# Performance work log

Hardware: AMD Instinct MI355X
Metric: run time of the kernel (lower is better)

## Reference

```python
import jax, jax.numpy as jnp
import numpy as np
import math

# dims matching init_kwargs
B, N, CS, CZ = 1, 512, 384, 128
H, C, PQ, PV = 8, 128, 8, 8
INF, EPS = 1e5, 1e-8

# ---- quaternion / motor helpers (PGA motor encoded as [qw,qx,qy,qz,tx,ty,tz,0]) ----

def quat_conj(q):
    return q * jnp.array([1.0, -1.0, -1.0, -1.0], q.dtype)

def quat_mul(a, b):
    aw, ax, ay, az = jnp.split(a, 4, -1)
    bw, bx, by, bz = jnp.split(b, 4, -1)
    return jnp.concatenate([
        aw*bw - ax*bx - ay*by - az*bz,
        aw*bx + ax*bw + ay*bz - az*by,
        aw*by - ax*bz + ay*bw + az*bx,
        aw*bz + ax*by - ay*bx + az*bw], -1)

def quat_rotate(q, v):
    qv = q[..., 1:]
    uv = jnp.cross(qv, v)
    uuv = jnp.cross(qv, uv)
    return v + 2.0 * (q[..., :1] * uv + uuv)

def point_trafo(p, q, t):
    # p [...,K,3]; rigid transform by frame motor, homogeneous 4-vector out
    pp = quat_rotate(q, p) + t
    return jnp.concatenate([pp, jnp.ones_like(pp[..., :1])], -1)

def mv_transform(mv, q, t):
    # versor sandwich on a 16-dim multivector: three rotatable 3-vector blocks,
    # the point block (7:10, weight at 10) also translates; slots 0 and 10:16 invariant
    s0 = mv[..., 0:1]
    v1 = quat_rotate(q, mv[..., 1:4])
    v2 = quat_rotate(q, mv[..., 4:7])
    w = mv[..., 10:11]
    p = quat_rotate(q, mv[..., 7:10]) + w * t
    return jnp.concatenate([s0, v1, v2, p, mv[..., 10:16]], -1)

def mv_transform_inv(mv, q, t):
    qc = quat_conj(q)
    s0 = mv[..., 0:1]
    v1 = quat_rotate(qc, mv[..., 1:4])
    v2 = quat_rotate(qc, mv[..., 4:7])
    w = mv[..., 10:11]
    p = quat_rotate(qc, mv[..., 7:10] - w * t)
    return jnp.concatenate([s0, v1, v2, p, mv[..., 10:16]], -1)


def _forward(s, g, z, T, mask, W_q, b_q, W_kv, b_kv, W_qp, b_qp, W_kp, b_kp,
             W_vg, b_vg, W_mg, W_b, b_b, W_dz, b_dz, head_weights,
             softmax_weights, W_out, b_out, W_geo):
    T8 = T[..., :8]                                      # extract_motor
    qn = T8[..., :4]
    qn = qn / jnp.sqrt(jnp.sum(qn**2, -1, keepdims=True) + EPS)
    tr = T8[..., 4:7]

    q = (s @ W_q + b_q).reshape(B, N, H, C)
    kv = (s @ W_kv + b_kv).reshape(B, N, H, 2 * C)
    k, v = kv[..., :C], kv[..., C:]

    def make_pts(W, bb):
        # split into 3 chunks + stack(dim=-1) == reshape(...,3,HP).swapaxes
        p = (s @ W + bb).reshape(B, N, 3, H * PQ).swapaxes(-1, -2)  # [B,N,HP,3]
        p4 = point_trafo(p, qn[:, :, None, :], tr[:, :, None, :])
        return p4.reshape(B, N, H, PQ, 4)

    q_pts = make_pts(W_qp, b_qp)
    k_pts = make_pts(W_kp, b_kp)

    v_g = (s @ W_vg + b_vg).reshape(B, N, PV, 16)
    v_g = jnp.einsum('oi,bnic->bnoc', W_mg,
                     jnp.concatenate([v_g, g], -2)).reshape(B, N, H, PV, 16)

    bias = jnp.einsum('bijz,zh->bhij', z, W_b) + b_b[None, :, None, None]
    a = jnp.einsum('bihc,bjhc->bhij', q, k) * math.sqrt(1.0 / (3 * C))
    a = a + math.sqrt(1.0 / 3.0) * bias

    disp = q_pts[:, :, None, :, :, :3] - k_pts[:, None, :, :, :, :3]  # [B,N,N,H,P,3]
    pt = jnp.sum(disp**2, -1)                                         # [B,N,N,H,P]
    hw = jax.nn.softplus(head_weights) * math.sqrt(1.0 / (3 * (PQ * 9.0 / 2)))
    pt = -0.5 * jnp.sum(pt * hw[None, None, None, :, None], -1)       # [B,N,N,H]

    sq_mask = INF * (mask[:, :, None] * mask[:, None, :] - 1.0)
    a = a + pt.transpose(0, 3, 1, 2) + sq_mask[:, None]
    a = jax.nn.softmax(softmax_weights[None, :, None, None] * a, axis=-1)

    o = jnp.einsum('bhij,bjhc->bihc', a, v)                           # [B,N,H,C]

    qb, tb = qn[:, :, None, None, :], tr[:, :, None, None, :]
    vg_glob = mv_transform(v_g, qb, tb)
    o_g = jnp.einsum('bhij,bjhpc->bihpc', a, vg_glob)
    o_g = mv_transform_inv(o_g, qb, tb)                               # [B,N,H,PV,16]
    n1 = jnp.sqrt(jnp.sum(o_g[..., :10]**2, -1) + EPS)
    n2 = jnp.sqrt(jnp.sum(o_g[..., 10:]**2, -1) + EPS)
    o_g_norm = jnp.stack([n1, n2], -1)                                # [B,N,H,PV,2]

    # local relative frame features (8 per head)
    q_rel = quat_mul(quat_conj(qn)[:, :, None, :], qn[:, None, :, :])
    t_rel = quat_rotate(quat_conj(qn)[:, :, None, :], tr[:, None, :, :] - tr[:, :, None, :])
    rel = jnp.concatenate([q_rel, t_rel, jnp.zeros_like(t_rel[..., :1])], -1)  # [B,N,N,8]
    o_rel = jnp.einsum('bhij,bijc->bihc', a, rel)

    o_pair = jnp.einsum('bhij,bijc->bihc', a, z @ W_dz + b_dz)        # [B,N,H,CZ//4]

    feats = jnp.concatenate([o_pair, o, o_rel,
                             o_g.reshape(B, N, H, PV * 16),
                             o_g_norm.reshape(B, N, H, PV * 2)], -1).reshape(B, N, -1)
    s_out = feats @ W_out + b_out                                     # [B,N,CS]
    g_out = jnp.einsum('oi,bnic->bnoc', W_geo, o_g.reshape(B, N, H * PV, 16))
    return s_out, g_out


def setup_inputs() -> dict:
    key = jax.random.key(0)
    ks = jax.random.split(key, 32)
    def rn(i, shape, sc=1.0):
        return sc * jax.random.normal(ks[i], shape, jnp.float32)
    s = rn(0, (B, N, CS))
    g = rn(1, (B, N, PV, 16))
    z = rn(2, (B, N, N, CZ))
    Traw = rn(3, (B, N, 16))
    qn = Traw[..., :4]
    qn = qn / jnp.sqrt(jnp.sum(qn**2, -1, keepdims=True) + 1e-8)
    T = Traw.at[..., :4].set(qn).at[..., 4:7].multiply(3.0).at[..., 7:].set(0.0)
    mask = jnp.ones((B, N), jnp.float32)
    w = 0.02
    CAT = H * (CZ // 4 + C + 8 + PV * 18)   # 2496
    return dict(
        s=s, g=g, z=z, T=T, mask=mask,
        W_q=rn(4, (CS, H * C), w), b_q=jnp.zeros((H * C,), jnp.float32),
        W_kv=rn(5, (CS, 2 * H * C), w), b_kv=jnp.zeros((2 * H * C,), jnp.float32),
        W_qp=rn(6, (CS, H * PQ * 3), w), b_qp=jnp.zeros((H * PQ * 3,), jnp.float32),
        W_kp=rn(7, (CS, H * PQ * 3), w), b_kp=jnp.zeros((H * PQ * 3,), jnp.float32),
        W_vg=rn(8, (CS, PV * 16), w), b_vg=jnp.zeros((PV * 16,), jnp.float32),
        W_mg=rn(9, (H * PV, 2 * PV), 0.1),
        W_b=rn(10, (CZ, H), w), b_b=jnp.zeros((H,), jnp.float32),
        W_dz=rn(11, (CZ, CZ // 4), w), b_dz=jnp.zeros((CZ // 4,), jnp.float32),
        head_weights=-2.0 + 0.3 * rn(12, (H,)),
        softmax_weights=jnp.ones((H,), jnp.float32) + 0.1 * rn(13, (H,)),
        W_out=rn(14, (CAT, CS), w), b_out=jnp.zeros((CS,), jnp.float32),
        W_geo=rn(15, (PV, H * PV), 0.1))


def reference(s, g, z, T, mask, W_q, b_q, W_kv, b_kv, W_qp, b_qp, W_kp, b_kp,
              W_vg, b_vg, W_mg, W_b, b_b, W_dz, b_dz, head_weights,
              softmax_weights, W_out, b_out, W_geo):
    return _forward(s, g, z, T, mask, W_q, b_q, W_kv, b_kv, W_qp, b_qp, W_kp,
                    b_kp, W_vg, b_vg, W_mg, W_b, b_b, W_dz, b_dz, head_weights,
                    softmax_weights, W_out, b_out, W_geo)
```

## Files before the change

kernel.cpp:

```cpp
#include <hip/hip_runtime.h>
#include <math.h>

#define NN 512
#define CSD 384
#define CZD 128
#define HD 8
#define CD 128
#define EPSV 1e-8f
#define INFV 100000.0f

#define OFF_QN    ((size_t)0)
#define OFF_TR    ((size_t)2048)
#define OFF_QSQ   ((size_t)3584)
#define OFF_KSQ   ((size_t)7680)
#define OFF_ROWT  ((size_t)11776)
#define OFF_COLT  ((size_t)15872)
#define OFF_SB    ((size_t)19968)
#define OFF_QBUF  ((size_t)52736)
#define OFF_KV    ((size_t)577024)
#define OFF_QPTS  ((size_t)1625600)
#define OFF_KPTS  ((size_t)1723904)
#define OFF_VGG   ((size_t)1822208)
#define OFF_ZB    ((size_t)2346496)
#define OFF_A     ((size_t)4443648)
#define OFF_X     ((size_t)6540800)
#define OFF_QPR   (OFF_X)
#define OFF_KPR   (OFF_X + 98304)
#define OFF_VGR   (OFF_X + 196608)
#define OFF_U     (OFF_X)
#define OFF_V     (OFF_X + 655360)
#define OFF_AZ    (OFF_X)
#define OFF_O     (OFF_X + 524288)
#define OFF_OG    (OFF_X + 1048576)
#define OFF_FEATS (OFF_X + 1572864)
#define OFF_VP    (OFF_ZB)

__device__ __forceinline__ void qrot(const float q[4], const float* v, float* out) {
    float qw = q[0], qx = q[1], qy = q[2], qz = q[3];
    float ux = qy*v[2] - qz*v[1];
    float uy = qz*v[0] - qx*v[2];
    float uz = qx*v[1] - qy*v[0];
    float uux = qy*uz - qz*uy;
    float uuy = qz*ux - qx*uz;
    float uuz = qx*uy - qy*ux;
    out[0] = v[0] + 2.0f*(qw*ux + uux);
    out[1] = v[1] + 2.0f*(qw*uy + uuy);
    out[2] = v[2] + 2.0f*(qw*uz + uuz);
}

__device__ __forceinline__ void gemm_tiles(const float* __restrict__ A, int lda,
                                           const float* __restrict__ B, int ldb,
                                           int m0, int n0, int k0, int nk,
                                           float acc[4][4], float* AsT, float* Bs) {
    int t = threadIdx.x;
    int tx = t & 15, ty = t >> 4;
    int arow = t >> 3, ak4 = (t & 7) << 2;
    int brow = t >> 4, bc4 = (t & 15) << 2;
    const float* Ap0 = A + (size_t)(m0 + arow)*lda + ak4;
    const float* Ap1 = A + (size_t)(m0 + arow + 32)*lda + ak4;
    const float* Bp0 = B + (size_t)brow*ldb + n0 + bc4;
    const float* Bp1 = B + (size_t)(brow + 16)*ldb + n0 + bc4;
    float4 a0 = *(const float4*)(Ap0 + k0);
    float4 a1 = *(const float4*)(Ap1 + k0);
    float4 b0 = *(const float4*)(Bp0 + (size_t)k0*ldb);
    float4 b1 = *(const float4*)(Bp1 + (size_t)k0*ldb);
    for (int kc = 0; kc < nk; kc++) {
        AsT[(ak4+0)*68 + arow] = a0.x;
        AsT[(ak4+1)*68 + arow] = a0.y;
        AsT[(ak4+2)*68 + arow] = a0.z;
        AsT[(ak4+3)*68 + arow] = a0.w;
        AsT[(ak4+0)*68 + arow+32] = a1.x;
        AsT[(ak4+1)*68 + arow+32] = a1.y;
        AsT[(ak4+2)*68 + arow+32] = a1.z;
        AsT[(ak4+3)*68 + arow+32] = a1.w;
        *(float4*)(Bs + brow*64 + bc4) = b0;
        *(float4*)(Bs + (brow+16)*64 + bc4) = b1;
        __syncthreads();
        if (kc + 1 < nk) {
            int kb = k0 + (kc+1)*32;
            a0 = *(const float4*)(Ap0 + kb);
            a1 = *(const float4*)(Ap1 + kb);
            b0 = *(const float4*)(Bp0 + (size_t)kb*ldb);
            b1 = *(const float4*)(Bp1 + (size_t)kb*ldb);
        }
        #pragma unroll
        for (int kk = 0; kk < 32; kk++) {
            float4 av = *(const float4*)(AsT + kk*68 + ty*4);
            float4 bv = *(const float4*)(Bs + kk*64 + tx*4);
            acc[0][0] += av.x*bv.x; acc[0][1] += av.x*bv.y; acc[0][2] += av.x*bv.z; acc[0][3] += av.x*bv.w;
            acc[1][0] += av.y*bv.x; acc[1][1] += av.y*bv.y; acc[1][2] += av.y*bv.z; acc[1][3] += av.y*bv.w;
            acc[2][0] += av.z*bv.x; acc[2][1] += av.z*bv.y; acc[2][2] += av.z*bv.z; acc[2][3] += av.z*bv.w;
            acc[3][0] += av.w*bv.x; acc[3][1] += av.w*bv.y; acc[3][2] += av.w*bv.z; acc[3][3] += av.w*bv.w;
        }
        __syncthreads();
    }
}

__device__ __forceinline__ void gemm_tiles_nt(const float* __restrict__ A,
                                              const float* __restrict__ B, int ldk,
                                              int m0, int n0, int nk,
                                              float acc[4][4], float* AsT, float* BsT) {
    int t = threadIdx.x;
    int tx = t & 15, ty = t >> 4;
    int arow = t >> 3, ak4 = (t & 7) << 2;
    const float* Ap0 = A + (size_t)(m0 + arow)*ldk + ak4;
    const float* Ap1 = A + (size_t)(m0 + arow + 32)*ldk + ak4;
    const float* Bp0 = B + (size_t)(n0 + arow)*ldk + ak4;
    const float* Bp1 = B + (size_t)(n0 + arow + 32)*ldk + ak4;
    float4 a0 = *(const float4*)(Ap0);
    float4 a1 = *(const float4*)(Ap1);
    float4 b0 = *(const float4*)(Bp0);
    float4 b1 = *(const float4*)(Bp1);
    for (int kc = 0; kc < nk; kc++) {
        AsT[(ak4+0)*68 + arow] = a0.x;
        AsT[(ak4+1)*68 + arow] = a0.y;
        AsT[(ak4+2)*68 + arow] = a0.z;
        AsT[(ak4+3)*68 + arow] = a0.w;
        AsT[(ak4+0)*68 + arow+32] = a1.x;
        AsT[(ak4+1)*68 + arow+32] = a1.y;
        AsT[(ak4+2)*68 + arow+32] = a1.z;
        AsT[(ak4+3)*68 + arow+32] = a1.w;
        BsT[(ak4+0)*68 + arow] = b0.x;
        BsT[(ak4+1)*68 + arow] = b0.y;
        BsT[(ak4+2)*68 + arow] = b0.z;
        BsT[(ak4+3)*68 + arow] = b0.w;
        BsT[(ak4+0)*68 + arow+32] = b1.x;
        BsT[(ak4+1)*68 + arow+32] = b1.y;
        BsT[(ak4+2)*68 + arow+32] = b1.z;
        BsT[(ak4+3)*68 + arow+32] = b1.w;
        __syncthreads();
        if (kc + 1 < nk) {
            int kb = (kc+1)*32;
            a0 = *(const float4*)(Ap0 + kb);
            a1 = *(const float4*)(Ap1 + kb);
            b0 = *(const float4*)(Bp0 + kb);
            b1 = *(const float4*)(Bp1 + kb);
        }
        #pragma unroll
        for (int kk = 0; kk < 32; kk++) {
            float4 av = *(const float4*)(AsT + kk*68 + ty*4);
            float4 bv = *(const float4*)(BsT + kk*68 + tx*4);
            acc[0][0] += av.x*bv.x; acc[0][1] += av.x*bv.y; acc[0][2] += av.x*bv.z; acc[0][3] += av.x*bv.w;
            acc[1][0] += av.y*bv.x; acc[1][1] += av.y*bv.y; acc[1][2] += av.y*bv.z; acc[1][3] += av.y*bv.w;
            acc[2][0] += av.z*bv.x; acc[2][1] += av.z*bv.y; acc[2][2] += av.z*bv.z; acc[2][3] += av.z*bv.w;
            acc[3][0] += av.w*bv.x; acc[3][1] += av.w*bv.y; acc[3][2] += av.w*bv.z; acc[3][3] += av.w*bv.w;
        }
        __syncthreads();
    }
}


__global__ void k_prep(const float* __restrict__ T, float* __restrict__ qn, float* __restrict__ tr) {
    int n = blockIdx.x*blockDim.x + threadIdx.x;
    if (n >= NN) return;
    float q0=T[n*16+0], q1=T[n*16+1], q2=T[n*16+2], q3=T[n*16+3];
    float inv = 1.0f/sqrtf(q0*q0+q1*q1+q2*q2+q3*q3 + EPSV);
    qn[n*4+0]=q0*inv; qn[n*4+1]=q1*inv; qn[n*4+2]=q2*inv; qn[n*4+3]=q3*inv;
    tr[n*3+0]=T[n*16+4]; tr[n*3+1]=T[n*16+5]; tr[n*3+2]=T[n*16+6];
}

__global__ __launch_bounds__(256) void k_proj_all(const float* __restrict__ s,
    const float* __restrict__ W_q,  const float* __restrict__ b_q,  float* __restrict__ qbuf,
    const float* __restrict__ W_kv, const float* __restrict__ b_kv, float* __restrict__ kvb,
    const float* __restrict__ W_qp, const float* __restrict__ b_qp, float* __restrict__ qpr,
    const float* __restrict__ W_kp, const float* __restrict__ b_kp, float* __restrict__ kpr,
    const float* __restrict__ W_vg, const float* __restrict__ b_vg, float* __restrict__ vgr) {
    __shared__ float AsT[32*68];
    __shared__ float Bs[32*64];
    int ny = blockIdx.y;
    const float* W; const float* bias; float* C; int N; int n0;
    if (ny < 16)      { W=W_q;  bias=b_q;  C=qbuf; N=1024; n0=ny*64; }
    else if (ny < 48) { W=W_kv; bias=b_kv; C=kvb;  N=2048; n0=(ny-16)*64; }
    else if (ny < 51) { W=W_qp; bias=b_qp; C=qpr;  N=192;  n0=(ny-48)*64; }
    else if (ny < 54) { W=W_kp; bias=b_kp; C=kpr;  N=192;  n0=(ny-51)*64; }
    else              { W=W_vg; bias=b_vg; C=vgr;  N=128;  n0=(ny-54)*64; }
    int m0 = blockIdx.x*64;
    float acc[4][4] = {};
    gemm_tiles(s, CSD, W, N, m0, n0, 0, 12, acc, AsT, Bs);
    int tx = threadIdx.x & 15, ty = threadIdx.x >> 4;
    float4 bb = *(const float4*)(bias + n0 + tx*4);
    #pragma unroll
    for (int rr = 0; rr < 4; rr++) {
        float4 o = make_float4(acc[rr][0]+bb.x, acc[rr][1]+bb.y, acc[rr][2]+bb.z, acc[rr][3]+bb.w);
        *(float4*)(C + (size_t)(m0+ty*4+rr)*N + n0 + tx*4) = o;
    }
}

__global__ __launch_bounds__(64) void k_geom(const float* __restrict__ qpr,
        const float* __restrict__ kpr, const float* __restrict__ vgr,
        const float* __restrict__ g, const float* __restrict__ W_mg,
        const float* __restrict__ qn, const float* __restrict__ tr,
        float* __restrict__ qpts, float* __restrict__ Qsq,
        float* __restrict__ kpts, float* __restrict__ Ksq, float* __restrict__ vgg) {
    int n = blockIdx.x, ny = blockIdx.y, m = threadIdx.x;
    float q[4] = {qn[n*4],qn[n*4+1],qn[n*4+2],qn[n*4+3]};
    float t0=tr[n*3], t1=tr[n*3+1], t2=tr[n*3+2];
    if (ny < 2) {
        const float* raw = ny ? kpr : qpr;
        float* pts = ny ? kpts : qpts;
        float* sq  = ny ? Ksq : Qsq;
        float p[3] = {raw[n*192 + m], raw[n*192 + 64 + m], raw[n*192 + 128 + m]};
        float r[3]; qrot(q,p,r);
        r[0]+=t0; r[1]+=t1; r[2]+=t2;
        pts[n*192+m*3+0]=r[0]; pts[n*192+m*3+1]=r[1]; pts[n*192+m*3+2]=r[2];
        float s = r[0]*r[0]+r[1]*r[1]+r[2]*r[2];
        s += __shfl_down(s,4,8);
        s += __shfl_down(s,2,8);
        s += __shfl_down(s,1,8);
        if ((m&7)==0) sq[n*8 + (m>>3)] = s;
    } else {
        int o = m;
        float in[16];
        #pragma unroll
        for (int c=0;c<16;c++){
            float acc=0.0f;
            #pragma unroll
            for (int i=0;i<8;i++)  acc += W_mg[o*16+i]*vgr[n*128+i*16+c];
            #pragma unroll
            for (int i=8;i<16;i++) acc += W_mg[o*16+i]*g[n*128+(i-8)*16+c];
            in[c]=acc;
        }
        float out[16];
        out[0]=in[0];
        qrot(q,in+1,out+1);
        qrot(q,in+4,out+4);
        float w=in[10];
        qrot(q,in+7,out+7);
        out[7]+=w*t0; out[8]+=w*t1; out[9]+=w*t2;
        #pragma unroll
        for (int c=10;c<16;c++) out[c]=in[c];
        #pragma unroll
        for (int c=0;c<16;c++) vgg[(size_t)n*1024+o*16+c]=out[c];
    }
}

__global__ __launch_bounds__(256) void k_uv(const float* __restrict__ qbuf, const float* __restrict__ kvb,
                    const float* __restrict__ qpts, const float* __restrict__ kpts,
                    const float* __restrict__ Qsq, const float* __restrict__ Ksq,
                    const float* __restrict__ hwraw, const float* __restrict__ b_b,
                    float* __restrict__ U, float* __restrict__ Vr,
                    float* __restrict__ rowt, float* __restrict__ colt) {
    int i = blockIdx.x; int t = threadIdx.x;
    #pragma unroll
    for (int h = 0; h < 8; h++) {
        float hw = log1pf(expf(hwraw[h])) * 0.09622504486493763f;
        if (t < 160) {
            float u, v;
            if (t < 128) {
                u = 0.05103103630798287f * qbuf[(size_t)i*1024 + h*128 + t];
                v = kvb[(size_t)i*2048 + h*256 + t];
            } else if (t < 152) {
                int d = t - 128;
                u = hw * qpts[i*192 + h*24 + d];
                v = kpts[i*192 + h*24 + d];
            } else { u = 0.0f; v = 0.0f; }
            U [((size_t)h*512 + i)*160 + t] = u;
            Vr[((size_t)h*512 + i)*160 + t] = v;
        }
        if (t == 160) rowt[h*512+i] = -0.5f*hw*Qsq[i*8+h] + 0.5773502691896258f*b_b[h] - INFV;
        if (t == 161) colt[h*512+i] = -0.5f*hw*Ksq[i*8+h];
    }
}

__global__ __launch_bounds__(128) void k_zb(const float* __restrict__ z,
        const float* __restrict__ W_b, float* __restrict__ zb) {
    __shared__ float zt[64*132];
    __shared__ float part[8*64];
    int i = blockIdx.x, j0 = blockIdx.y*64;
    int t = threadIdx.x;
    #pragma unroll
    for (int l = 0; l < 16; l++) {
        int f = t + l*128;
        int row = f >> 5, c4 = (f & 31) << 2;
        float4 v = *(const float4*)(z + ((size_t)(i*NN) + j0 + row)*CZD + c4);
        *(float4*)(zt + row*132 + c4) = v;
    }
    __syncthreads();
    int w = t >> 6, j = t & 63;
    int cbase = w*64;
    float acc[8] = {};
    #pragma unroll
    for (int c16 = 0; c16 < 16; c16++) {
        float4 v = *(const float4*)(zt + j*132 + cbase + c16*4);
        int c = cbase + c16*4;
        #pragma unroll
        for (int h = 0; h < 8; h++)
            acc[h] += v.x*W_b[(c+0)*8+h] + v.y*W_b[(c+1)*8+h]
                    + v.z*W_b[(c+2)*8+h] + v.w*W_b[(c+3)*8+h];
    }
    if (w == 1) {
        #pragma unroll
        for (int h = 0; h < 8; h++) part[h*64 + j] = acc[h];
    }
    __syncthreads();
    if (w == 0) {
        #pragma unroll
        for (int h = 0; h < 8; h++)
            zb[((size_t)h*512 + i)*512 + j0 + j] = acc[h] + part[h*64 + j];
    }
}

__global__ __launch_bounds__(256) void k_scorefill(const float* __restrict__ U, const float* __restrict__ Vr,
        const float* __restrict__ rowt, const float* __restrict__ colt,
        const float* __restrict__ zb, const float* __restrict__ mask,
        const float* __restrict__ sw, float* __restrict__ Am) {
    __shared__ float AsT[32*68];
    __shared__ float BsT[32*68];
    int h = blockIdx.z;
    int m0 = blockIdx.x*64, n0 = blockIdx.y*64;
    float acc[4][4] = {};
    gemm_tiles_nt(U + (size_t)h*512*160, Vr + (size_t)h*512*160, 160, m0, n0, 5, acc, AsT, BsT);
    int tx = threadIdx.x & 15, ty = threadIdx.x >> 4;
    float swh = sw[h];
    float4 ct = *(const float4*)(colt + h*512 + n0 + tx*4);
    float4 mj = *(const float4*)(mask + n0 + tx*4);
    #pragma unroll
    for (int rr = 0; rr < 4; rr++) {
        int i = m0 + ty*4 + rr;
        float rt = rowt[h*512 + i];
        float mi = mask[i] * INFV;
        float4 zv = *(const float4*)(zb + ((size_t)h*512 + i)*512 + n0 + tx*4);
        float4 r;
        r.x = (acc[rr][0] + rt + ct.x + 0.5773502691896258f*zv.x + mi*mj.x)*swh;
        r.y = (acc[rr][1] + rt + ct.y + 0.5773502691896258f*zv.y + mi*mj.y)*swh;
        r.z = (acc[rr][2] + rt + ct.z + 0.5773502691896258f*zv.z + mi*mj.z)*swh;
        r.w = (acc[rr][3] + rt + ct.w + 0.5773502691896258f*zv.w + mi*mj.w)*swh;
        *(float4*)(Am + ((size_t)h*512 + i)*512 + n0 + tx*4) = r;
    }
}

__global__ __launch_bounds__(256) void k_pack(const float* __restrict__ kvb,
        const float* __restrict__ vgg, float* __restrict__ Vp) {
    int idx = blockIdx.x*256 + threadIdx.x;
    int c4 = idx & 63, j = (idx >> 6) & 511, h = idx >> 15;
    int col = c4*4;
    float4 v;
    if (col < 128) v = *(const float4*)(kvb + (size_t)j*2048 + h*256 + 128 + col);
    else           v = *(const float4*)(vgg + (size_t)j*1024 + h*128 + col - 128);
    *(float4*)(Vp + ((size_t)h*512 + j)*256 + col) = v;
}

__global__ __launch_bounds__(256) void k_softmax(float* __restrict__ Am,
        const float* __restrict__ qn, const float* __restrict__ tr, float* __restrict__ S) {
    __shared__ float red[8];
    __shared__ float sred[4][8];
    int row = blockIdx.x;
    float* p = Am + (size_t)row*512;
    int t = threadIdx.x;
    float x0 = p[t], x1 = p[t+256];
    float m = fmaxf(x0, x1);
    #pragma unroll
    for (int o = 32; o > 0; o >>= 1) m = fmaxf(m, __shfl_xor(m, o));
    int wv = t >> 6, ln = t & 63;
    if (ln == 0) red[wv] = m;
    __syncthreads();
    m = fmaxf(fmaxf(red[0], red[1]), fmaxf(red[2], red[3]));
    float e0 = expf(x0 - m), e1 = expf(x1 - m);
    float sm = e0 + e1;
    #pragma unroll
    for (int o = 32; o > 0; o >>= 1) sm += __shfl_xor(sm, o);
    __syncthreads();
    if (ln == 0) red[4 + wv] = sm;
    __syncthreads();
    float inv = 1.0f / (red[4]+red[5]+red[6]+red[7]);
    float a0 = e0*inv, a1 = e1*inv;
    p[t] = a0;
    p[t+256] = a1;
    float4 q0 = *(const float4*)(qn + t*4);
    float4 q1 = *(const float4*)(qn + (t+256)*4);
    float acc[8];
    acc[0] = a0*q0.x + a1*q1.x;
    acc[1] = a0*q0.y + a1*q1.y;
    acc[2] = a0*q0.z + a1*q1.z;
    acc[3] = a0*q0.w + a1*q1.w;
    acc[4] = a0*tr[t*3+0] + a1*tr[(t+256)*3+0];
    acc[5] = a0*tr[t*3+1] + a1*tr[(t+256)*3+1];
    acc[6] = a0*tr[t*3+2] + a1*tr[(t+256)*3+2];
    acc[7] = a0 + a1;
    #pragma unroll
    for (int c = 0; c < 8; c++) {
        #pragma unroll
        for (int o = 32; o > 0; o >>= 1) acc[c] += __shfl_xor(acc[c], o);
    }
    if (ln == 0) {
        #pragma unroll
        for (int c = 0; c < 8; c++) sred[wv][c] = acc[c];
    }
    __syncthreads();
    if (t < 8) {
        int h = row >> 9, i = row & 511;
        S[i*64 + h*8 + t] = sred[0][t]+sred[1][t]+sred[2][t]+sred[3][t];
    }
}

__global__ __launch_bounds__(256) void k_apply(const float* __restrict__ Am,
        const float* __restrict__ Vp, float* __restrict__ obuf, float* __restrict__ og) {
    __shared__ float AsT[32*68];
    __shared__ float Bs[32*64];
    int m0 = blockIdx.x*64;
    int n0 = blockIdx.y*64;
    int h = blockIdx.z & 7, js = blockIdx.z >> 3;
    float acc[4][4] = {};
    gemm_tiles(Am + (size_t)h*512*512, 512, Vp + (size_t)h*512*256, 256,
               m0, n0, js*128, 4, acc, AsT, Bs);
    int tx = threadIdx.x & 15, ty = threadIdx.x >> 4;
    float* base = (n0 < 128) ? (obuf + h*128 + n0) : (og + h*128 + n0 - 128);
    #pragma unroll
    for (int rr = 0; rr < 4; rr++) {
        #pragma unroll
        for (int cc = 0; cc < 4; cc++)
            atomicAdd(base + (size_t)(m0+ty*4+rr)*1024 + tx*4 + cc, acc[rr][cc]);
    }
}

__global__ __launch_bounds__(128) void k_az(const float* __restrict__ Am,
        const float* __restrict__ z, float* __restrict__ az) {
    __shared__ float aT[128*8];
    int i = blockIdx.x, j0 = blockIdx.y*128, t = threadIdx.x;
    #pragma unroll
    for (int l = 0; l < 8; l++) {
        int f = t + l*128;
        int h = f >> 7, jl = f & 127;
        aT[jl*8 + h] = Am[((size_t)h*512 + i)*512 + j0 + jl];
    }
    __syncthreads();
    float acc[8] = {};
    const float* zp = z + ((size_t)i*NN + j0)*CZD + t;
    for (int jl = 0; jl < 128; jl++) {
        float zv = zp[(size_t)jl*CZD];
        float4 a0 = *(const float4*)(aT + jl*8);
        float4 a1 = *(const float4*)(aT + jl*8 + 4);
        acc[0] += a0.x*zv; acc[1] += a0.y*zv; acc[2] += a0.z*zv; acc[3] += a0.w*zv;
        acc[4] += a1.x*zv; acc[5] += a1.y*zv; acc[6] += a1.z*zv; acc[7] += a1.w*zv;
    }
    #pragma unroll
    for (int h = 0; h < 8; h++)
        atomicAdd(az + (size_t)i*1024 + h*128 + t, acc[h]);
}

__global__ __launch_bounds__(256) void k_finalize(const float* __restrict__ obuf,
        const float* __restrict__ az, const float* __restrict__ W_dz,
        const float* __restrict__ b_dz, float* __restrict__ og,
        const float* __restrict__ S, const float* __restrict__ qn,
        const float* __restrict__ tr, float* __restrict__ feats) {
    __shared__ float azs[1024];
    __shared__ float wdz[4096];
    int i = blockIdx.x, t = threadIdx.x;
    float* fb = feats + (size_t)i*2496;
    for (int idx = t; idx < 1024; idx += 256) {
        azs[idx] = az[(size_t)i*1024 + idx];
        int h = idx >> 7, c = idx & 127;
        fb[h*312 + 32 + c] = obuf[(size_t)i*1024 + idx];
    }
    for (int idx = t; idx < 4096; idx += 256) wdz[idx] = W_dz[idx];
    __syncthreads();
    {
        int h = t >> 5, m = t & 31;
        float acc = b_dz[m];
        #pragma unroll 8
        for (int zc = 0; zc < 128; zc++) acc += azs[h*128+zc]*wdz[zc*32+m];
        fb[h*312 + m] = acc;
    }
    float qc[4] = {qn[i*4], -qn[i*4+1], -qn[i*4+2], -qn[i*4+3]};
    float t0 = tr[i*3], t1 = tr[i*3+1], t2 = tr[i*3+2];
    if (t < 64) {
        int h = t >> 3, p = t & 7;
        float* f = fb + h*312;
        float* ogp = og + (size_t)i*1024 + h*128 + p*16;
        float in[16];
        #pragma unroll
        for (int c=0;c<16;c++) in[c]=ogp[c];
        float out[16];
        out[0]=in[0];
        qrot(qc,in+1,out+1);
        qrot(qc,in+4,out+4);
        float w=in[10];
        float tmp[3]={in[7]-w*t0, in[8]-w*t1, in[9]-w*t2};
        qrot(qc,tmp,out+7);
        #pragma unroll
        for (int c2=10;c2<16;c2++) out[c2]=in[c2];
        float n1=EPSV, n2=EPSV;
        #pragma unroll
        for (int c2=0;c2<10;c2++) n1 += out[c2]*out[c2];
        #pragma unroll
        for (int c2=10;c2<16;c2++) n2 += out[c2]*out[c2];
        n1=sqrtf(n1); n2=sqrtf(n2);
        #pragma unroll
        for (int c2=0;c2<16;c2++){ f[168+p*16+c2]=out[c2]; ogp[c2]=out[c2]; }
        f[296+p*2]=n1; f[296+p*2+1]=n2;
    } else if (t < 72) {
        int h = t - 64;
        float* f = fb + h*312;
        const float* Sr = S + i*64 + h*8;
        float b0=Sr[0], b1=Sr[1], b2=Sr[2], b3=Sr[3];
        f[160] = qc[0]*b0 - qc[1]*b1 - qc[2]*b2 - qc[3]*b3;
        f[161] = qc[0]*b1 + qc[1]*b0 + qc[2]*b3 - qc[3]*b2;
        f[162] = qc[0]*b2 - qc[1]*b3 + qc[2]*b0 + qc[3]*b1;
        f[163] = qc[0]*b3 + qc[1]*b2 - qc[2]*b1 + qc[3]*b0;
        float A = Sr[7];
        float v[3]={Sr[4]-A*t0, Sr[5]-A*t1, Sr[6]-A*t2};
        float r[3]; qrot(qc,v,r);
        f[164]=r[0]; f[165]=r[1]; f[166]=r[2]; f[167]=0.0f;
    }
}

__global__ __launch_bounds__(256) void k_gout(const float* __restrict__ og, const float* __restrict__ W_geo,
                       float* __restrict__ gout) {
    int idx = blockIdx.x*blockDim.x+threadIdx.x;
    int c = idx & 15;
    int o = (idx>>4) & 7;
    int n = idx >> 7;
    float acc=0.0f;
    #pragma unroll 4
    for (int i2=0;i2<64;i2++) acc += W_geo[o*64+i2]*og[(size_t)n*1024 + i2*16 + c];
    gout[(size_t)n*128 + o*16 + c]=acc;
}

__global__ __launch_bounds__(256) void k_sout(const float* __restrict__ feats,
        const float* __restrict__ W_out, const float* __restrict__ b_out, float* __restrict__ out) {
    __shared__ float AsT[32*68];
    __shared__ float Bs[32*64];
    int m0 = blockIdx.x*64, n0 = blockIdx.y*64, kz = blockIdx.z;
    float acc[4][4] = {};
    gemm_tiles(feats, 2496, W_out, CSD, m0, n0, kz*192, 6, acc, AsT, Bs);
    int tx = threadIdx.x & 15, ty = threadIdx.x >> 4;
    #pragma unroll
    for (int rr = 0; rr < 4; rr++) {
        #pragma unroll
        for (int cc = 0; cc < 4; cc++) {
            float v = acc[rr][cc];
            if (kz == 0) v += b_out[n0 + tx*4 + cc];
            atomicAdd(out + (size_t)(m0+ty*4+rr)*CSD + n0 + tx*4 + cc, v);
        }
    }
}


extern "C" void kernel_launch(void* const* d_in, const int* in_sizes, int n_in,
                              void* d_out, int out_size, void* d_ws, size_t ws_size,
                              hipStream_t stream) {
    const float* s     = (const float*)d_in[0];
    const float* g     = (const float*)d_in[1];
    const float* z     = (const float*)d_in[2];
    const float* T     = (const float*)d_in[3];
    const float* mask  = (const float*)d_in[4];
    const float* W_q   = (const float*)d_in[5];
    const float* b_q   = (const float*)d_in[6];
    const float* W_kv  = (const float*)d_in[7];
    const float* b_kv  = (const float*)d_in[8];
    const float* W_qp  = (const float*)d_in[9];
    const float* b_qp  = (const float*)d_in[10];
    const float* W_kp  = (const float*)d_in[11];
    const float* b_kp  = (const float*)d_in[12];
    const float* W_vg  = (const float*)d_in[13];
    const float* b_vg  = (const float*)d_in[14];
    const float* W_mg  = (const float*)d_in[15];
    const float* W_b   = (const float*)d_in[16];
    const float* b_b   = (const float*)d_in[17];
    const float* W_dz  = (const float*)d_in[18];
    const float* b_dz  = (const float*)d_in[19];
    const float* hw    = (const float*)d_in[20];
    const float* sw    = (const float*)d_in[21];
    const float* W_out = (const float*)d_in[22];
    const float* b_out = (const float*)d_in[23];
    const float* W_geo = (const float*)d_in[24];

    float* ws   = (float*)d_ws;
    float* out  = (float*)d_out;

    float* qn   = ws + OFF_QN;
    float* tr   = ws + OFF_TR;
    float* Qsq  = ws + OFF_QSQ;
    float* Ksq  = ws + OFF_KSQ;
    float* rowt = ws + OFF_ROWT;
    float* colt = ws + OFF_COLT;
    float* Sbuf = ws + OFF_SB;
    float* qbuf = ws + OFF_QBUF;
    float* kvb  = ws + OFF_KV;
    float* qpts = ws + OFF_QPTS;
    float* kpts = ws + OFF_KPTS;
    float* vgg  = ws + OFF_VGG;
    float* zb   = ws + OFF_ZB;
    float* Am   = ws + OFF_A;
    float* qpr  = ws + OFF_QPR;
    float* kpr  = ws + OFF_KPR;
    float* vgr  = ws + OFF_VGR;
    float* U    = ws + OFF_U;
    float* Vr   = ws + OFF_V;
    float* az   = ws + OFF_AZ;
    float* obuf = ws + OFF_O;
    float* og   = ws + OFF_OG;
    float* feats= ws + OFF_FEATS;
    float* Vp   = ws + OFF_VP;

    k_prep<<<2,256,0,stream>>>(T,qn,tr);
    k_proj_all<<<dim3(8,56),256,0,stream>>>(s, W_q,b_q,qbuf, W_kv,b_kv,kvb,
                                            W_qp,b_qp,qpr, W_kp,b_kp,kpr, W_vg,b_vg,vgr);
    k_geom<<<dim3(NN,3),64,0,stream>>>(qpr,kpr,vgr,g,W_mg,qn,tr,qpts,Qsq,kpts,Ksq,vgg);
    k_uv<<<NN,256,0,stream>>>(qbuf,kvb,qpts,kpts,Qsq,Ksq,hw,b_b,U,Vr,rowt,colt);
    k_zb<<<dim3(NN,8),128,0,stream>>>(z,W_b,zb);
    k_scorefill<<<dim3(8,8,8),256,0,stream>>>(U,Vr,rowt,colt,zb,mask,sw,Am);
    k_pack<<<1024,256,0,stream>>>(kvb,vgg,Vp);
    hipMemsetAsync(ws + OFF_X, 0, (size_t)3*512*1024*sizeof(float), stream);
    k_softmax<<<4096,256,0,stream>>>(Am,qn,tr,Sbuf);
    k_apply<<<dim3(8,4,32),256,0,stream>>>(Am,Vp,obuf,og);
    k_az<<<dim3(NN,4),128,0,stream>>>(Am,z,az);
    k_finalize<<<NN,256,0,stream>>>(obuf,az,W_dz,b_dz,og,Sbuf,qn,tr,feats);
    k_gout<<<256,256,0,stream>>>(og,W_geo,out + (size_t)NN*CSD);
    hipMemsetAsync(out, 0, (size_t)NN*CSD*sizeof(float), stream);
    k_sout<<<dim3(8,6,13),256,0,stream>>>(feats,W_out,b_out,out);
}
```

Before: 489.5 us.

## Pre-project pair features through W_dz before attention-weighted pair aggregation

The pair-bias kernel now also projects z through W_dz (128 to 32 channels) while it reads z, storing a compact zd buffer. The attention-weighted pair aggregation then reads zd instead of full z, which replaces the second full pass over the large z tensor with a quarter-size read. The projection moves out of finalize and atomics for az are removed. The k_apply split-K is halved from four chunks to two, reducing atomic traffic at the cost of fewer blocks.

After: 505.1 us. 3.2% more time.

```diff
diff --git a/kernel.cpp b/kernel.cpp
--- a/kernel.cpp
+++ b/kernel.cpp
@@ -29,11 +29,11 @@
 #define OFF_VGR   (OFF_X + 196608)
 #define OFF_U     (OFF_X)
 #define OFF_V     (OFF_X + 655360)
-#define OFF_AZ    (OFF_X)
 #define OFF_O     (OFF_X + 524288)
 #define OFF_OG    (OFF_X + 1048576)
 #define OFF_FEATS (OFF_X + 1572864)
 #define OFF_VP    (OFF_ZB)
+#define OFF_ZD    ((size_t)9437184)
 
 __device__ __forceinline__ void qrot(const float q[4], const float* v, float* out) {
     float qw = q[0], qx = q[1], qy = q[2], qz = q[3];
@@ -262,42 +262,33 @@
     }
 }
 
-__global__ __launch_bounds__(128) void k_zb(const float* __restrict__ z,
-        const float* __restrict__ W_b, float* __restrict__ zb) {
-    __shared__ float zt[64*132];
-    __shared__ float part[8*64];
-    int i = blockIdx.x, j0 = blockIdx.y*64;
-    int t = threadIdx.x;
-    #pragma unroll
-    for (int l = 0; l < 16; l++) {
-        int f = t + l*128;
-        int row = f >> 5, c4 = (f & 31) << 2;
-        float4 v = *(const float4*)(z + ((size_t)(i*NN) + j0 + row)*CZD + c4);
-        *(float4*)(zt + row*132 + c4) = v;
-    }
-    __syncthreads();
-    int w = t >> 6, j = t & 63;
-    int cbase = w*64;
-    float acc[8] = {};
-    #pragma unroll
-    for (int c16 = 0; c16 < 16; c16++) {
-        float4 v = *(const float4*)(zt + j*132 + cbase + c16*4);
-        int c = cbase + c16*4;
-        #pragma unroll
-        for (int h = 0; h < 8; h++)
-            acc[h] += v.x*W_b[(c+0)*8+h] + v.y*W_b[(c+1)*8+h]
-                    + v.z*W_b[(c+2)*8+h] + v.w*W_b[(c+3)*8+h];
-    }
-    if (w == 1) {
-        #pragma unroll
-        for (int h = 0; h < 8; h++) part[h*64 + j] = acc[h];
-    }
-    __syncthreads();
-    if (w == 0) {
-        #pragma unroll
-        for (int h = 0; h < 8; h++)
-            zb[((size_t)h*512 + i)*512 + j0 + j] = acc[h] + part[h*64 + j];
-    }
+__global__ __launch_bounds__(128) void k_zpre(const float* __restrict__ z,
+        const float* __restrict__ W_b, const float* __restrict__ W_dz,
+        float* __restrict__ zb, float* __restrict__ zd) {
+    int i = blockIdx.x, j = blockIdx.y*128 + threadIdx.x;
+    const float* zr = z + ((size_t)i*NN + j)*CZD;
+    float accb[8] = {};
+    float accd[32] = {};
+    for (int k0 = 0; k0 < 128; k0 += 32) {
+        float zreg[32];
+        #pragma unroll
+        for (int q = 0; q < 8; q++)
+            *(float4*)(zreg + q*4) = *(const float4*)(zr + k0 + q*4);
+        #pragma unroll
+        for (int k = 0; k < 32; k++) {
+            float zv = zreg[k];
+            int kk = k0 + k;
+            #pragma unroll
+            for (int h = 0; h < 8; h++) accb[h] += zv * W_b[kk*8 + h];
+            #pragma unroll
+            for (int m = 0; m < 32; m++) accd[m] += zv * W_dz[kk*32 + m];
+        }
+    }
+    #pragma unroll
+    for (int h = 0; h < 8; h++) zb[((size_t)h*512 + i)*512 + j] = accb[h];
+    #pragma unroll
+    for (int q = 0; q < 8; q++)
+        *(float4*)(zd + ((size_t)i*512 + j)*32 + q*4) = *(const float4*)(accd + q*4);
 }
 
 __global__ __launch_bounds__(256) void k_scorefill(const float* __restrict__ U, const float* __restrict__ Vr,
@@ -402,7 +393,7 @@
     int h = blockIdx.z & 7, js = blockIdx.z >> 3;
     float acc[4][4] = {};
     gemm_tiles(Am + (size_t)h*512*512, 512, Vp + (size_t)h*512*256, 256,
-               m0, n0, js*128, 4, acc, AsT, Bs);
+               m0, n0, js*256, 8, acc, AsT, Bs);
     int tx = threadIdx.x & 15, ty = threadIdx.x >> 4;
     float* base = (n0 < 128) ? (obuf + h*128 + n0) : (og + h*128 + n0 - 128);
     #pragma unroll
@@ -413,53 +404,54 @@
     }
 }
 
-__global__ __launch_bounds__(128) void k_az(const float* __restrict__ Am,
-        const float* __restrict__ z, float* __restrict__ az) {
-    __shared__ float aT[128*8];
-    int i = blockIdx.x, j0 = blockIdx.y*128, t = threadIdx.x;
-    #pragma unroll
-    for (int l = 0; l < 8; l++) {
-        int f = t + l*128;
-        int h = f >> 7, jl = f & 127;
-        aT[jl*8 + h] = Am[((size_t)h*512 + i)*512 + j0 + jl];
+__global__ __launch_bounds__(256) void k_opair(const float* __restrict__ Am,
+        const float* __restrict__ zd, const float* __restrict__ b_dz,
+        float* __restrict__ feats) {
+    __shared__ float aT[8*516];
+    __shared__ float part[3*64*4];
+    int i = blockIdx.x, t = threadIdx.x;
+    #pragma unroll
+    for (int l = 0; l < 16; l++) {
+        int f = t + l*256; int h = f >> 9, j = f & 511;
+        aT[h*516 + j] = Am[((size_t)h*512 + i)*512 + j];
     }
     __syncthreads();
-    float acc[8] = {};
-    const float* zp = z + ((size_t)i*NN + j0)*CZD + t;
+    int js = t >> 6, h = (t >> 3) & 7, mq = t & 7;
+    const float* zp = zd + ((size_t)i*512 + js*128)*32 + mq*4;
+    const float* ar = aT + h*516 + js*128;
+    float4 acc = make_float4(0.0f,0.0f,0.0f,0.0f);
+    #pragma unroll 4
     for (int jl = 0; jl < 128; jl++) {
-        float zv = zp[(size_t)jl*CZD];
-        float4 a0 = *(const float4*)(aT + jl*8);
-        float4 a1 = *(const float4*)(aT + jl*8 + 4);
-        acc[0] += a0.x*zv; acc[1] += a0.y*zv; acc[2] += a0.z*zv; acc[3] += a0.w*zv;
-        acc[4] += a1.x*zv; acc[5] += a1.y*zv; acc[6] += a1.z*zv; acc[7] += a1.w*zv;
-    }
-    #pragma unroll
-    for (int h = 0; h < 8; h++)
-        atomicAdd(az + (size_t)i*1024 + h*128 + t, acc[h]);
+        float av = ar[jl];
+        float4 zv = *(const float4*)(zp + jl*32);
+        acc.x += av*zv.x; acc.y += av*zv.y; acc.z += av*zv.z; acc.w += av*zv.w;
+    }
+    if (js > 0) *(float4*)(part + ((js-1)*64 + (t & 63))*4) = acc;
+    __syncthreads();
+    if (js == 0) {
+        int idx = t & 63;
+        #pragma unroll
+        for (int q = 1; q < 4; q++) {
+            float4 p = *(const float4*)(part + ((q-1)*64 + idx)*4);
+            acc.x += p.x; acc.y += p.y; acc.z += p.z; acc.w += p.w;
+        }
+        float4 bb = *(const float4*)(b_dz + mq*4);
+        float* f = feats + (size_t)i*2496 + h*312 + mq*4;
+        f[0] = acc.x + bb.x; f[1] = acc.y + bb.y; f[2] = acc.z + bb.z; f[3] = acc.w + bb.w;
+    }
 }
 
 __global__ __launch_bounds__(256) void k_finalize(const float* __restrict__ obuf,
-        const float* __restrict__ az, const float* __restrict__ W_dz,
-        const float* __restrict__ b_dz, float* __restrict__ og,
-        const float* __restrict__ S, const float* __restrict__ qn,
-        const float* __restrict__ tr, float* __restrict__ feats) {
-    __shared__ float azs[1024];
-    __shared__ float wdz[4096];
+        float* __restrict__ og, const float* __restrict__ S,
+        const float* __restrict__ qn, const float* __restrict__ tr,
+        float* __restrict__ feats) {
     int i = blockIdx.x, t = threadIdx.x;
     float* fb = feats + (size_t)i*2496;
-    for (int idx = t; idx < 1024; idx += 256) {
-        azs[idx] = az[(size_t)i*1024 + idx];
+    #pragma unroll
+    for (int l = 0; l < 4; l++) {
+        int idx = t + l*256;
         int h = idx >> 7, c = idx & 127;
         fb[h*312 + 32 + c] = obuf[(size_t)i*1024 + idx];
-    }
-    for (int idx = t; idx < 4096; idx += 256) wdz[idx] = W_dz[idx];
-    __syncthreads();
-    {
-        int h = t >> 5, m = t & 31;
-        float acc = b_dz[m];
-        #pragma unroll 8
-        for (int zc = 0; zc < 128; zc++) acc += azs[h*128+zc]*wdz[zc*32+m];
-        fb[h*312 + m] = acc;
     }
     float qc[4] = {qn[i*4], -qn[i*4+1], -qn[i*4+2], -qn[i*4+3]};
     float t0 = tr[i*3], t1 = tr[i*3+1], t2 = tr[i*3+2];
@@ -587,25 +579,25 @@
     float* vgr  = ws + OFF_VGR;
     float* U    = ws + OFF_U;
     float* Vr   = ws + OFF_V;
-    float* az   = ws + OFF_AZ;
     float* obuf = ws + OFF_O;
     float* og   = ws + OFF_OG;
     float* feats= ws + OFF_FEATS;
     float* Vp   = ws + OFF_VP;
+    float* zd   = ws + OFF_ZD;
 
     k_prep<<<2,256,0,stream>>>(T,qn,tr);
     k_proj_all<<<dim3(8,56),256,0,stream>>>(s, W_q,b_q,qbuf, W_kv,b_kv,kvb,
                                             W_qp,b_qp,qpr, W_kp,b_kp,kpr, W_vg,b_vg,vgr);
     k_geom<<<dim3(NN,3),64,0,stream>>>(qpr,kpr,vgr,g,W_mg,qn,tr,qpts,Qsq,kpts,Ksq,vgg);
     k_uv<<<NN,256,0,stream>>>(qbuf,kvb,qpts,kpts,Qsq,Ksq,hw,b_b,U,Vr,rowt,colt);
-    k_zb<<<dim3(NN,8),128,0,stream>>>(z,W_b,zb);
+    k_zpre<<<dim3(NN,4),128,0,stream>>>(z,W_b,W_dz,zb,zd);
     k_scorefill<<<dim3(8,8,8),256,0,stream>>>(U,Vr,rowt,colt,zb,mask,sw,Am);
     k_pack<<<1024,256,0,stream>>>(kvb,vgg,Vp);
-    hipMemsetAsync(ws + OFF_X, 0, (size_t)3*512*1024*sizeof(float), stream);
+    hipMemsetAsync(ws + OFF_O, 0, (size_t)2*512*1024*sizeof(float), stream);
     k_softmax<<<4096,256,0,stream>>>(Am,qn,tr,Sbuf);
-    k_apply<<<dim3(8,4,32),256,0,stream>>>(Am,Vp,obuf,og);
-    k_az<<<dim3(NN,4),128,0,stream>>>(Am,z,az);
-    k_finalize<<<NN,256,0,stream>>>(obuf,az,W_dz,b_dz,og,Sbuf,qn,tr,feats);
+    k_apply<<<dim3(8,4,16),256,0,stream>>>(Am,Vp,obuf,og);
+    k_opair<<<NN,256,0,stream>>>(Am,zd,b_dz,feats);
+    k_finalize<<<NN,256,0,stream>>>(obuf,og,Sbuf,qn,tr,feats);
     k_gout<<<256,256,0,stream>>>(og,W_geo,out + (size_t)NN*CSD);
     hipMemsetAsync(out, 0, (size_t)NN*CSD*sizeof(float), stream);
     k_sout<<<dim3(8,6,13),256,0,stream>>>(feats,W_out,b_out,out);
```
